# Kernel optimization log

Measured on AMD Instinct MI355X. Metric: run time of the kernel, lower is better.

Reference implementation:

```python
import jax, jax.numpy as jnp
import numpy as np

B, C_IN, C_OUT, H, W, K = 8, 64, 64, 64, 64, 9
T = H * W  # 4096 tokens
EPS = 1e-12  # F.normalize eps


def setup_inputs() -> dict:
    key = jax.random.key(0)
    ks = jax.random.split(key, 7)
    x = jax.random.normal(ks[0], (B, C_IN, H, W), dtype=jnp.float32)
    Wq = jax.random.normal(ks[1], (T, T), dtype=jnp.float32) * 0.02
    Wk = jax.random.normal(ks[2], (T, T), dtype=jnp.float32) * 0.02
    Wv = jax.random.normal(ks[3], (T, T), dtype=jnp.float32) * 0.02
    Wo = jax.random.normal(ks[4], (T, T), dtype=jnp.float32) * 0.02
    conv_w = jax.random.normal(ks[5], (C_OUT, C_IN, K), dtype=jnp.float32) * 0.05
    conv_b = jax.random.normal(ks[6], (C_OUT,), dtype=jnp.float32) * 0.01
    return {"x": x, "Wq": Wq, "Wk": Wk, "Wv": Wv, "Wo": Wo,
            "conv_w": conv_w, "conv_b": conv_b}


def reference(x, Wq, Wk, Wv, Wo, conv_w, conv_b):
    Bq, Cc, Hh, Ww = x.shape
    Tt = Hh * Ww
    xf = x.reshape(Bq, Cc, Tt)  # flatten(start_dim=2)
    # nn.Linear over the token (last) dim: y[...,s] = sum_t x[...,t] * W[s,t]
    q = jnp.einsum('bct,st->bcs', xf, Wq)
    k = jnp.einsum('bct,st->bcs', xf, Wk)
    v = jnp.einsum('bct,st->bcs', xf, Wv)
    # cosine similarity over channel dim (dim=1), clamp to >= 0
    kn = k / jnp.maximum(jnp.linalg.norm(k, axis=1, keepdims=True), EPS)
    qn = q / jnp.maximum(jnp.linalg.norm(q, axis=1, keepdims=True), EPS)
    sim = jnp.clip(jnp.einsum('bct,bcs->bts', kn, qn), 0.0, None)  # [B,T,T]
    # top-K most similar neighbors per token (largest=True for similarity)
    _, idx = jax.lax.top_k(sim, K)  # [B,T,K] int32
    # gather neighbor values: prime[b,c,t,j] = v[b,c,idx[b,t,j]]
    gather = jax.vmap(lambda vv, ii: vv[:, ii])  # vv:[C,T], ii:[T,K] -> [C,T,K]
    prime = gather(v, idx).reshape(Bq, Cc, Tt * K)
    # Conv1d(kernel=K, stride=K, padding=0): aggregates each K-neighbor group
    out = jax.lax.conv_general_dilated(
        prime, conv_w, window_strides=(K,), padding='VALID',
        dimension_numbers=('NCH', 'OIH', 'NCH'))  # [B,C_OUT,T]
    out = out + conv_b[None, :, None]
    out = jnp.einsum('bct,st->bcs', out, Wo)  # w_o over token dim
    return out.reshape(Bq, conv_w.shape[0], Hh, Ww)
```

## Files before the change

### kernel.cpp

```cpp
#include <hip/hip_runtime.h>

#define T4096 4096
#define CH 64

__global__ __launch_bounds__(256) void gemm_qkv(
    const float* __restrict__ X,
    const float* __restrict__ Wq, const float* __restrict__ Wk, const float* __restrict__ Wv,
    float* __restrict__ QT, float* __restrict__ KT, float* __restrict__ VT)
{
    const float* W = (blockIdx.z == 0) ? Wq : (blockIdx.z == 1) ? Wk : Wv;
    float*       O = (blockIdx.z == 0) ? QT : (blockIdx.z == 1) ? KT : VT;
    const int b  = blockIdx.y;
    const int s0 = blockIdx.x * 128;

    __shared__ float As[64][132];
    __shared__ float Bs[64][68];

    const int tid = threadIdx.x;
    const int tx = tid & 15;   const int c0 = tx * 4;
    const int my = tid >> 4;   const int m0 = my * 8;
    const int lr = tid >> 3;
    const int lk = (tid & 7) * 4;
    const int sw = lk;

    float acc[8][4];
#pragma unroll
    for (int i = 0; i < 8; ++i)
#pragma unroll
        for (int j = 0; j < 4; ++j) acc[i][j] = 0.f;

    const float* Xb = X + (size_t)b * CH * T4096;

    for (int k0 = 0; k0 < T4096; k0 += 64) {
#pragma unroll
        for (int kk = 0; kk < 2; ++kk) {
            const int kb = 32 * kk + lk;
#pragma unroll
            for (int p = 0; p < 4; ++p) {
                int row = lr + 32 * p;
                float4 v = *(const float4*)(W + (size_t)(s0 + row) * T4096 + k0 + kb);
                int col = row ^ sw;
                As[kb + 0][col] = v.x; As[kb + 1][col] = v.y;
                As[kb + 2][col] = v.z; As[kb + 3][col] = v.w;
            }
#pragma unroll
            for (int p = 0; p < 2; ++p) {
                int row = lr + 32 * p;
                float4 v = *(const float4*)(Xb + (size_t)row * T4096 + k0 + kb);
                int col = row ^ sw;
                Bs[kb + 0][col] = v.x; Bs[kb + 1][col] = v.y;
                Bs[kb + 2][col] = v.z; Bs[kb + 3][col] = v.w;
            }
        }
        __syncthreads();
#pragma unroll
        for (int k = 0; k < 64; ++k) {
            const int swk = k & 28;
            float4 a0 = *(const float4*)&As[k][(m0) ^ swk];
            float4 a1 = *(const float4*)&As[k][(m0 + 4) ^ swk];
            float4 bv = *(const float4*)&Bs[k][c0 ^ swk];
            float am[8] = {a0.x,a0.y,a0.z,a0.w,a1.x,a1.y,a1.z,a1.w};
            float bn[4] = {bv.x,bv.y,bv.z,bv.w};
#pragma unroll
            for (int i = 0; i < 8; ++i)
#pragma unroll
                for (int j = 0; j < 4; ++j) acc[i][j] = fmaf(am[i], bn[j], acc[i][j]);
        }
        __syncthreads();
    }
    if (blockIdx.z == 0) {
#pragma unroll
        for (int i = 0; i < 8; ++i) {
            *(float4*)(O + ((size_t)(b * 16 + tx) * T4096 + s0 + m0 + i) * 4) =
                make_float4(acc[i][0], acc[i][1], acc[i][2], acc[i][3]);
        }
    } else {
#pragma unroll
        for (int i = 0; i < 8; ++i) {
            *(float4*)(O + ((size_t)b * T4096 + s0 + m0 + i) * CH + c0) =
                make_float4(acc[i][0], acc[i][1], acc[i][2], acc[i][3]);
        }
    }
}

__global__ __launch_bounds__(256) void normalize_qk(float* __restrict__ QT, float* __restrict__ KT)
{
    int gtok = blockIdx.x * 4 + (threadIdx.x >> 6);
    int lane = threadIdx.x & 63;
    bool isQ = (gtok < 8 * T4096);
    int t = gtok & (T4096 - 1);
    int b = (gtok >> 12) & 7;
    float* p;
    if (isQ) p = QT + ((size_t)(b * 16 + (lane >> 2)) * T4096 + t) * 4 + (lane & 3);
    else     p = KT + ((size_t)b * T4096 + t) * CH + lane;
    float v = *p;
    float ss = v * v;
#pragma unroll
    for (int off = 32; off; off >>= 1) ss += __shfl_xor(ss, off);
    float n = fmaxf(sqrtf(ss), 1e-12f);
    *p = v / n;
}

__global__ __launch_bounds__(512) void sim_topk(
    const float* __restrict__ Qr, const float* __restrict__ KT, int* __restrict__ IDX)
{
    const int wg = blockIdx.x;
    const int b  = wg & 7;
    const int t0 = (wg >> 3) * 32;

    __shared__ float Kn[32][68];

    const int tid = threadIdx.x;
    const int tx = tid & 31;
    const int ty = tid >> 5;

    {
        int row = tid >> 4; int cc = (tid & 15) * 4;
        *(float4*)&Kn[row][cc] =
            *(const float4*)(KT + ((size_t)b * T4096 + t0 + row) * CH + cc);
    }
    __syncthreads();

    float tv[2][9]; int ti[2][9];
#pragma unroll
    for (int r = 0; r < 2; ++r)
#pragma unroll
        for (int q = 0; q < 9; ++q) { tv[r][q] = -1.f; ti[r][q] = 0x7fffffff; }

    const float* qbase = Qr + ((size_t)b * 16 * T4096 + tx) * 4;

    for (int s0 = 0; s0 < T4096; s0 += 64) {
        float acc[2][2];
        acc[0][0] = acc[0][1] = acc[1][0] = acc[1][1] = 0.f;

        const float* qp = qbase + (size_t)s0 * 4;
#pragma unroll 2
        for (int c4g = 0; c4g < 16; ++c4g) {
            float4 q0 = *(const float4*)(qp + (size_t)c4g * (T4096 * 4));
            float4 q1 = *(const float4*)(qp + (size_t)c4g * (T4096 * 4) + 128);
            float4 k0 = *(const float4*)&Kn[ty][c4g * 4];
            float4 k1 = *(const float4*)&Kn[16 + ty][c4g * 4];
            acc[0][0] = fmaf(k0.x, q0.x, acc[0][0]); acc[0][0] = fmaf(k0.y, q0.y, acc[0][0]);
            acc[0][0] = fmaf(k0.z, q0.z, acc[0][0]); acc[0][0] = fmaf(k0.w, q0.w, acc[0][0]);
            acc[0][1] = fmaf(k0.x, q1.x, acc[0][1]); acc[0][1] = fmaf(k0.y, q1.y, acc[0][1]);
            acc[0][1] = fmaf(k0.z, q1.z, acc[0][1]); acc[0][1] = fmaf(k0.w, q1.w, acc[0][1]);
            acc[1][0] = fmaf(k1.x, q0.x, acc[1][0]); acc[1][0] = fmaf(k1.y, q0.y, acc[1][0]);
            acc[1][0] = fmaf(k1.z, q0.z, acc[1][0]); acc[1][0] = fmaf(k1.w, q0.w, acc[1][0]);
            acc[1][1] = fmaf(k1.x, q1.x, acc[1][1]); acc[1][1] = fmaf(k1.y, q1.y, acc[1][1]);
            acc[1][1] = fmaf(k1.z, q1.z, acc[1][1]); acc[1][1] = fmaf(k1.w, q1.w, acc[1][1]);
        }

#pragma unroll
        for (int rr = 0; rr < 2; ++rr)
#pragma unroll
            for (int cc = 0; cc < 2; ++cc) {
                float v = fmaxf(acc[rr][cc], 0.f);
                int s = s0 + tx + 32 * cc;
                if (v > tv[rr][8] || (v == tv[rr][8] && s < ti[rr][8])) {
                    float cv = v; int ci = s;
#pragma unroll
                    for (int p = 0; p < 9; ++p) {
                        bool better = (cv > tv[rr][p]) || (cv == tv[rr][p] && ci < ti[rr][p]);
                        if (better) {
                            float ov = tv[rr][p]; int oi = ti[rr][p];
                            tv[rr][p] = cv; ti[rr][p] = ci; cv = ov; ci = oi;
                        }
                    }
                }
            }
    }

#pragma unroll
    for (int rr = 0; rr < 2; ++rr) {
        float mv[9]; int mi[9];
#pragma unroll
        for (int q = 0; q < 9; ++q) { mv[q] = tv[rr][q]; mi[q] = ti[rr][q]; }
        const int outrow = t0 + rr * 16 + ty;
        int* dst = IDX + ((size_t)b * T4096 + outrow) * 9;
        for (int sel = 0; sel < 9; ++sel) {
            float bv = mv[0]; int bi = mi[0]; int bl = tx;
#pragma unroll
            for (int m = 1; m < 32; m <<= 1) {
                float ov = __shfl_xor(bv, m);
                int   oi = __shfl_xor(bi, m);
                int   ol = __shfl_xor(bl, m);
                if (ov > bv || (ov == bv && oi < bi)) { bv = ov; bi = oi; bl = ol; }
            }
            if (tx == 0) dst[sel] = bi;
            if (tx == bl) {
#pragma unroll
                for (int q = 0; q < 8; ++q) { mv[q] = mv[q + 1]; mi[q] = mi[q + 1]; }
                mv[8] = -2.f; mi[8] = 0x7fffffff;
            }
        }
    }
}

__global__ void transpose_w(const float* __restrict__ cw, float* __restrict__ wT3)
{
    int idx = blockIdx.x * 256 + threadIdx.x;
    if (idx >= 64 * 64 * 9) return;
    int q   = idx & 3;
    int o   = (idx >> 2) & 63;
    int i4g = (idx >> 8) & 15;
    int j   = idx >> 12;
    wT3[idx] = cw[o * 576 + (i4g * 4 + q) * 9 + j];
}

__global__ __launch_bounds__(256) void gather_conv(
    const float* __restrict__ VT, const int* __restrict__ IDX,
    const float* __restrict__ wT3, const float* __restrict__ conv_b,
    float* __restrict__ out1)
{
    const int b  = blockIdx.y;
    const int w  = threadIdx.x >> 6;
    const int o  = threadIdx.x & 63;
    const int t0 = (blockIdx.x * 4 + w) * 4;

    __shared__ float vv[4][4][9][64];
    __shared__ int   nb[4][36];

    if (o < 36) nb[w][o] = IDX[((size_t)b * T4096 + t0) * 9 + o];
    __syncthreads();

#pragma unroll
    for (int tok = 0; tok < 4; ++tok)
#pragma unroll
        for (int j = 0; j < 9; ++j) {
            int n = nb[w][tok * 9 + j];
            vv[w][tok][j][o] = VT[((size_t)b * T4096 + n) * CH + o];
        }
    __syncthreads();

    float cb = conv_b[o];
    float a0 = cb, a1 = cb, a2 = cb, a3 = cb;
    for (int j = 0; j < 9; ++j) {
#pragma unroll
        for (int i4 = 0; i4 < 16; ++i4) {
            float4 w4 = *(const float4*)(wT3 + (((size_t)j * 16 + i4) * 64 + o) * 4);
            float4 v0 = *(const float4*)&vv[w][0][j][i4 * 4];
            float4 v1 = *(const float4*)&vv[w][1][j][i4 * 4];
            float4 v2 = *(const float4*)&vv[w][2][j][i4 * 4];
            float4 v3 = *(const float4*)&vv[w][3][j][i4 * 4];
            a0 = fmaf(v0.x, w4.x, a0); a0 = fmaf(v0.y, w4.y, a0); a0 = fmaf(v0.z, w4.z, a0); a0 = fmaf(v0.w, w4.w, a0);
            a1 = fmaf(v1.x, w4.x, a1); a1 = fmaf(v1.y, w4.y, a1); a1 = fmaf(v1.z, w4.z, a1); a1 = fmaf(v1.w, w4.w, a1);
            a2 = fmaf(v2.x, w4.x, a2); a2 = fmaf(v2.y, w4.y, a2); a2 = fmaf(v2.z, w4.z, a2); a2 = fmaf(v2.w, w4.w, a2);
            a3 = fmaf(v3.x, w4.x, a3); a3 = fmaf(v3.y, w4.y, a3); a3 = fmaf(v3.z, w4.z, a3); a3 = fmaf(v3.w, w4.w, a3);
        }
    }
    out1[((size_t)b * T4096 + t0 + 0) * CH + o] = a0;
    out1[((size_t)b * T4096 + t0 + 1) * CH + o] = a1;
    out1[((size_t)b * T4096 + t0 + 2) * CH + o] = a2;
    out1[((size_t)b * T4096 + t0 + 3) * CH + o] = a3;
}

__global__ __launch_bounds__(256) void gemm_out(
    const float* __restrict__ out1, const float* __restrict__ Wo, float* __restrict__ Out)
{
    const int b  = blockIdx.y;
    const int s0 = blockIdx.x * 128;
    __shared__ float As[32][68];
    __shared__ float Bs[32][132];
    const int tid = threadIdx.x;
    const int tx = tid & 15;  const int sl = tx * 8;
    const int my = tid >> 4;  const int c0 = my * 4;
    const int lr = tid >> 3;
    const int lk = (tid & 7) * 4;
    const int sw = lk;

    float acc[4][8];
#pragma unroll
    for (int i = 0; i < 4; ++i)
#pragma unroll
        for (int j = 0; j < 8; ++j) acc[i][j] = 0.f;

    for (int k0 = 0; k0 < T4096; k0 += 32) {
        {
            int r  = tid >> 3;
            int cL = (tid & 7) * 8;
            const float* src = out1 + ((size_t)b * T4096 + k0 + r) * CH + cL;
            *(float4*)&As[r][cL]     = *(const float4*)(src);
            *(float4*)&As[r][cL + 4] = *(const float4*)(src + 4);
        }
#pragma unroll
        for (int p = 0; p < 4; ++p) {
            int row = lr + 32 * p;
            float4 v = *(const float4*)(Wo + (size_t)(s0 + row) * T4096 + k0 + lk);
            int col = row ^ sw;
            Bs[lk + 0][col] = v.x; Bs[lk + 1][col] = v.y;
            Bs[lk + 2][col] = v.z; Bs[lk + 3][col] = v.w;
        }
        __syncthreads();
#pragma unroll
        for (int k = 0; k < 32; ++k) {
            const int swk = k & 28;
            float4 a  = *(const float4*)&As[k][c0];
            float4 b0 = *(const float4*)&Bs[k][(sl) ^ swk];
            float4 b1 = *(const float4*)&Bs[k][(sl + 4) ^ swk];
            float av[4] = {a.x, a.y, a.z, a.w};
            float bv[8] = {b0.x,b0.y,b0.z,b0.w,b1.x,b1.y,b1.z,b1.w};
#pragma unroll
            for (int i = 0; i < 4; ++i)
#pragma unroll
                for (int j = 0; j < 8; ++j) acc[i][j] = fmaf(av[i], bv[j], acc[i][j]);
        }
        __syncthreads();
    }
#pragma unroll
    for (int i = 0; i < 4; ++i) {
        float* dst = Out + ((size_t)b * CH + c0 + i) * T4096 + s0 + sl;
        *(float4*)dst       = make_float4(acc[i][0], acc[i][1], acc[i][2], acc[i][3]);
        *(float4*)(dst + 4) = make_float4(acc[i][4], acc[i][5], acc[i][6], acc[i][7]);
    }
}

extern "C" void kernel_launch(void* const* d_in, const int* in_sizes, int n_in,
                              void* d_out, int out_size, void* d_ws, size_t ws_size,
                              hipStream_t stream)
{
    const float* x  = (const float*)d_in[0];
    const float* Wq = (const float*)d_in[1];
    const float* Wk = (const float*)d_in[2];
    const float* Wv = (const float*)d_in[3];
    const float* Wo = (const float*)d_in[4];
    const float* cw = (const float*)d_in[5];
    const float* cb = (const float*)d_in[6];
    float* Out = (float*)d_out;

    char* ws = (char*)d_ws;
    float* QT   = (float*)(ws);
    float* KT   = (float*)(ws + (size_t)8  * 1024 * 1024);
    float* VT   = (float*)(ws + (size_t)16 * 1024 * 1024);
    int*   IDXb = (int*)  (ws + (size_t)24 * 1024 * 1024);
    float* wT3  = (float*)(ws + (size_t)26 * 1024 * 1024);
    float* out1 = QT;

    gemm_qkv<<<dim3(32, 8, 3), dim3(256), 0, stream>>>(x, Wq, Wk, Wv, QT, KT, VT);
    normalize_qk<<<dim3(16384), dim3(256), 0, stream>>>(QT, KT);
    sim_topk<<<dim3(1024), dim3(512), 0, stream>>>(QT, KT, IDXb);
    transpose_w<<<dim3(144), dim3(256), 0, stream>>>(cw, wT3);
    gather_conv<<<dim3(256, 8), dim3(256), 0, stream>>>(VT, IDXb, wT3, cb, out1);
    gemm_out<<<dim3(32, 8), dim3(256), 0, stream>>>(out1, Wo, Out);
}
```

Measured before the change: 1.795 ms.

## Pack top-k keys into u64, share row thresholds, and block Q layout

Top-k candidates are now packed into single 64-bit keys (float bits in the high word, inverted index in the low word), so insertion becomes a branchless compare-swap chain. The insert threshold is a warp-wide maximum of the per-lane 9th-best key, refreshed only when some lane inserted, which skips more candidates early. The normalized Q buffer is re-laid out in 64-token blocks so each block's channel groups sit contiguously, and the channel loop is fully unrolled. This trades more shuffles and 64-bit registers for fewer divergent insertions and more local Q loads.

```diff
diff --git a/kernel.cpp b/kernel.cpp
--- a/kernel.cpp
+++ b/kernel.cpp
@@ -2,6 +2,7 @@
 
 #define T4096 4096
 #define CH 64
+typedef unsigned long long u64;
 
 __global__ __launch_bounds__(256) void gemm_qkv(
     const float* __restrict__ X,
@@ -71,7 +72,8 @@
     if (blockIdx.z == 0) {
 #pragma unroll
         for (int i = 0; i < 8; ++i) {
-            *(float4*)(O + ((size_t)(b * 16 + tx) * T4096 + s0 + m0 + i) * 4) =
+            int s = s0 + m0 + i;
+            *(float4*)(O + ((((size_t)b * 64 + (s >> 6)) * 16 + tx) * 64 + (s & 63)) * 4) =
                 make_float4(acc[i][0], acc[i][1], acc[i][2], acc[i][3]);
         }
     } else {
@@ -91,7 +93,7 @@
     int t = gtok & (T4096 - 1);
     int b = (gtok >> 12) & 7;
     float* p;
-    if (isQ) p = QT + ((size_t)(b * 16 + (lane >> 2)) * T4096 + t) * 4 + (lane & 3);
+    if (isQ) p = QT + ((((size_t)b * 64 + (t >> 6)) * 16 + (lane >> 2)) * 64 + (t & 63)) * 4 + (lane & 3);
     else     p = KT + ((size_t)b * T4096 + t) * CH + lane;
     float v = *p;
     float ss = v * v;
@@ -121,23 +123,24 @@
     }
     __syncthreads();
 
-    float tv[2][9]; int ti[2][9];
+    u64 tv[2][9];
 #pragma unroll
     for (int r = 0; r < 2; ++r)
 #pragma unroll
-        for (int q = 0; q < 9; ++q) { tv[r][q] = -1.f; ti[r][q] = 0x7fffffff; }
-
-    const float* qbase = Qr + ((size_t)b * 16 * T4096 + tx) * 4;
-
-    for (int s0 = 0; s0 < T4096; s0 += 64) {
+        for (int q = 0; q < 9; ++q) tv[r][q] = 0ULL;
+    u64 thr[2] = {0ULL, 0ULL};
+
+    const float* qb0 = Qr + ((size_t)b * 64 * 1024 + tx) * 4;
+
+    for (int blk = 0; blk < 64; ++blk) {
+        const float* bp = qb0 + (size_t)blk * 4096;
         float acc[2][2];
         acc[0][0] = acc[0][1] = acc[1][0] = acc[1][1] = 0.f;
 
-        const float* qp = qbase + (size_t)s0 * 4;
-#pragma unroll 2
+#pragma unroll
         for (int c4g = 0; c4g < 16; ++c4g) {
-            float4 q0 = *(const float4*)(qp + (size_t)c4g * (T4096 * 4));
-            float4 q1 = *(const float4*)(qp + (size_t)c4g * (T4096 * 4) + 128);
+            float4 q0 = *(const float4*)(bp + c4g * 256);
+            float4 q1 = *(const float4*)(bp + c4g * 256 + 128);
             float4 k0 = *(const float4*)&Kn[ty][c4g * 4];
             float4 k1 = *(const float4*)&Kn[16 + ty][c4g * 4];
             acc[0][0] = fmaf(k0.x, q0.x, acc[0][0]); acc[0][0] = fmaf(k0.y, q0.y, acc[0][0]);
@@ -150,47 +153,61 @@
             acc[1][1] = fmaf(k1.z, q1.z, acc[1][1]); acc[1][1] = fmaf(k1.w, q1.w, acc[1][1]);
         }
 
+        bool ins = false;
+        const int sb = blk * 64 + tx;
 #pragma unroll
         for (int rr = 0; rr < 2; ++rr)
 #pragma unroll
             for (int cc = 0; cc < 2; ++cc) {
                 float v = fmaxf(acc[rr][cc], 0.f);
-                int s = s0 + tx + 32 * cc;
-                if (v > tv[rr][8] || (v == tv[rr][8] && s < ti[rr][8])) {
-                    float cv = v; int ci = s;
+                int s = sb + 32 * cc;
+                u64 key = ((u64)__float_as_uint(v) << 32) | (u64)(4095 - s);
+                if (key > thr[rr]) {
+                    u64 cv = key;
 #pragma unroll
                     for (int p = 0; p < 9; ++p) {
-                        bool better = (cv > tv[rr][p]) || (cv == tv[rr][p] && ci < ti[rr][p]);
-                        if (better) {
-                            float ov = tv[rr][p]; int oi = ti[rr][p];
-                            tv[rr][p] = cv; ti[rr][p] = ci; cv = ov; ci = oi;
-                        }
+                        u64 t  = tv[rr][p];
+                        bool g = cv > t;
+                        tv[rr][p] = g ? cv : t;
+                        cv        = g ? t  : cv;
                     }
+                    ins = true;
                 }
             }
+        if (__any(ins)) {
+#pragma unroll
+            for (int r = 0; r < 2; ++r) {
+                u64 m = tv[r][8];
+#pragma unroll
+                for (int msk = 1; msk < 32; msk <<= 1) {
+                    u64 o = __shfl_xor(m, msk);
+                    if (o > m) m = o;
+                }
+                thr[r] = m;
+            }
+        }
     }
 
 #pragma unroll
     for (int rr = 0; rr < 2; ++rr) {
-        float mv[9]; int mi[9];
-#pragma unroll
-        for (int q = 0; q < 9; ++q) { mv[q] = tv[rr][q]; mi[q] = ti[rr][q]; }
+        u64 mv[9];
+#pragma unroll
+        for (int q = 0; q < 9; ++q) mv[q] = tv[rr][q];
         const int outrow = t0 + rr * 16 + ty;
         int* dst = IDX + ((size_t)b * T4096 + outrow) * 9;
         for (int sel = 0; sel < 9; ++sel) {
-            float bv = mv[0]; int bi = mi[0]; int bl = tx;
+            u64 bk = mv[0]; int bl = tx;
 #pragma unroll
             for (int m = 1; m < 32; m <<= 1) {
-                float ov = __shfl_xor(bv, m);
-                int   oi = __shfl_xor(bi, m);
-                int   ol = __shfl_xor(bl, m);
-                if (ov > bv || (ov == bv && oi < bi)) { bv = ov; bi = oi; bl = ol; }
-            }
-            if (tx == 0) dst[sel] = bi;
+                u64 ok = __shfl_xor(bk, m);
+                int ol = __shfl_xor(bl, m);
+                if (ok > bk) { bk = ok; bl = ol; }
+            }
+            if (tx == 0) dst[sel] = 4095 - (int)(unsigned)bk;
             if (tx == bl) {
 #pragma unroll
-                for (int q = 0; q < 8; ++q) { mv[q] = mv[q + 1]; mi[q] = mi[q + 1]; }
-                mv[8] = -2.f; mi[8] = 0x7fffffff;
+                for (int q = 0; q < 8; ++q) mv[q] = mv[q + 1];
+                mv[8] = 0ULL;
             }
         }
     }
```

New measurement: 3.162 ms. +76.2%, slower.
